# Kernel tuning notes

Hardware: AMD Instinct MI355X
Metric: run time of the kernel (lower is better)

The kernel has to match this reference:

```python
import jax, jax.numpy as jnp
import numpy as np

B, C, H, W = 1, 128, 48, 48
HC = 32                     # head_channel
NH = C // HC                # num heads = 4
K = 16                      # n_clusters
N = H * W                   # 2304
SCALE = HC ** 0.5
EPS = 1e-6


def setup_inputs() -> dict:
    key = jax.random.key(0)
    ks = jax.random.split(key, 20)
    s = 0.05  # weight init scale ~ xavier-ish for C=128
    def g(i, shape, sc=s):
        return jax.random.normal(ks[i], shape, dtype=jnp.float32) * sc
    return {
        'q_img': g(0, (B, C, H, W), 1.0),
        'k_img_map': g(1, (B, C, H, W), 1.0),
        'v_img_map': g(2, (B, C, H, W), 1.0),
        'pixel_coefficients': jax.random.uniform(ks[3], (B, N, N), dtype=jnp.float32),
        'labels': jax.random.randint(ks[4], (B, H, W), 0, K),
        # projections (stored as [in, out]; y = x @ w + b)
        'wq': g(5, (C, C)), 'bq': jnp.zeros((C,), jnp.float32),
        'wk': g(6, (C, C)), 'bk': jnp.zeros((C,), jnp.float32),
        'wv': g(7, (C, C)), 'bv': jnp.zeros((C,), jnp.float32),
        # mlp_1: Linear(C,2C) -> LeakyReLU(0.01) -> Linear(2C,C) (dropout=0 -> identity)
        'w1a': g(8, (C, 2 * C)), 'b1a': jnp.zeros((2 * C,), jnp.float32),
        'w1b': g(9, (2 * C, C)), 'b1b': jnp.zeros((C,), jnp.float32),
        # mlp_2
        'w2a': g(10, (C, 2 * C)), 'b2a': jnp.zeros((2 * C,), jnp.float32),
        'w2b': g(11, (2 * C, C)), 'b2b': jnp.zeros((C,), jnp.float32),
    }


def _mlp(x, wa, ba, wb, bb):
    h = x @ wa + ba
    h = jax.nn.leaky_relu(h, negative_slope=0.01)
    return h @ wb + bb


def reference(q_img, k_img_map, v_img_map, pixel_coefficients,
              wq, bq, wk, bk, wv, bv,
              w1a, b1a, w1b, b1b, w2a, b2a, w2b, b2b,
              labels):
    # projections on channel-last pixels
    q = q_img.transpose(0, 2, 3, 1).reshape(B, N, C) @ wq + bq
    k = k_img_map.transpose(0, 2, 3, 1).reshape(B, N, C) @ wk + bk
    v = v_img_map.transpose(0, 2, 3, 1).reshape(B, N, C) @ wv + bv

    labels_flat = labels.reshape(B, N)
    onehot = jax.nn.one_hot(labels_flat, K, dtype=q.dtype)        # [B,N,K]
    num_k = jnp.einsum('bnk,bnc->bkc', onehot, k)                 # [B,K,C]
    den_k = onehot.sum(axis=1)[:, :, None] + EPS                  # [B,K,1]
    centers_k = num_k / den_k

    qm = q.reshape(B, N, NH, HC).transpose(0, 2, 1, 3)            # [B,h,N,d]
    km = k.reshape(B, N, NH, HC).transpose(0, 2, 1, 3)
    vm = v.reshape(B, N, NH, HC).transpose(0, 2, 1, 3)
    kcm = centers_k.reshape(B, K, NH, HC).transpose(0, 2, 1, 3)   # [B,h,K,d]

    attn_intra = jnp.einsum('bhid,bhjd->bhij', qm, km)            # [B,h,N,N]
    attn_centers = jnp.einsum('bhid,bhkd->bhik', qm, kcm)         # [B,h,N,K]

    # gather center score per key's cluster: attn_centers[b,h,i,labels[b,j]]
    idx = jnp.broadcast_to(labels_flat[:, None, None, :], (B, NH, N, N))
    attn_inter = jnp.take_along_axis(attn_centers, idx, axis=3)   # [B,h,N,N]
    attn_inter = attn_inter * pixel_coefficients[:, None, :, :]

    same = labels_flat[:, None, :, None] == labels_flat[:, None, None, :]  # [B,1,N,N]
    scores = jnp.where(same, attn_intra, attn_inter) / SCALE
    attn_w = jax.nn.softmax(scores, axis=-1)

    out = jnp.einsum('bhij,bhjd->bhid', attn_w, vm)
    out = out.transpose(0, 2, 1, 3).reshape(B, N, C)              # [B,N,C]

    v_spatial = v.reshape(B, H, W, C).transpose(0, 3, 1, 2)       # [B,C,H,W]
    rs1 = v_spatial + _mlp(out, w1a, b1a, w1b, b1b).transpose(0, 2, 1).reshape(B, C, H, W)
    rs1_flat = rs1.transpose(0, 2, 3, 1).reshape(B, N, C)
    rs2 = rs1 + _mlp(rs1_flat, w2a, b2a, w2b, b2b).transpose(0, 2, 1).reshape(B, C, H, W)
    return rs2
```

## Files before the change

### kernel.cpp

```cpp
#include <hip/hip_runtime.h>
#include <hip/hip_bf16.h>
#include <math.h>

#define NPIX 2304
#define CCH  128
#define NH   4
#define HC   32
#define NCL  16
#define KSPLIT 8
#define KEYS 288
#define NSTEP 9
#define QSCALE 0.25503489f
#define PPT  16

typedef __attribute__((ext_vector_type(8))) short short8;
typedef __attribute__((ext_vector_type(4))) short short4v;
typedef __attribute__((ext_vector_type(4))) float f32x4;

#if __has_builtin(__builtin_amdgcn_exp2f)
#define EXP2(x) __builtin_amdgcn_exp2f(x)
#else
#define EXP2(x) __expf((x) * 0.6931471805599453f)
#endif

static __device__ __forceinline__ short f2bf(float x) {
    __hip_bfloat16 b = __float2bfloat16(x);
    return *reinterpret_cast<short*>(&b);
}

__global__ void __launch_bounds__(256) pack_w_kernel(
        const float* __restrict__ wq,  const float* __restrict__ wk,
        const float* __restrict__ wv,
        const float* __restrict__ w1a, const float* __restrict__ w1b,
        const float* __restrict__ w2a, const float* __restrict__ w2b,
        float4* __restrict__ pq,  float4* __restrict__ pk,
        float4* __restrict__ pv,
        short* __restrict__ t1a, short* __restrict__ t1b,
        short* __restrict__ t2a, short* __restrict__ t2b) {
    const int idx = blockIdx.x * 256 + threadIdx.x;
    if (idx < 12288) {
        const int which = idx >> 12, local = idx & 4095;
        const float* src = (which == 0) ? wq : (which == 1) ? wk : wv;
        float4*      dst = (which == 0) ? pq : (which == 1) ? pk : pv;
        const int g = local >> 7, o = local & 127;
        float4 v;
        v.x = src[(4 * g + 0) * 128 + o];
        v.y = src[(4 * g + 1) * 128 + o];
        v.z = src[(4 * g + 2) * 128 + o];
        v.w = src[(4 * g + 3) * 128 + o];
        dst[local] = v;
    } else {
        const int i2 = idx - 12288;
        const int which = i2 >> 12, local = i2 & 4095;
        short8 s;
        if (which == 0 || which == 2) {
            const float* src = (which == 0) ? w1a : w2a;
            short*       dst = (which == 0) ? t1a : t2a;
            const int o = local >> 4, g = local & 15;
#pragma unroll
            for (int j = 0; j < 8; ++j) s[j] = f2bf(src[(g * 8 + j) * 256 + o]);
            *(short8*)(dst + (size_t)o * 128 + g * 8) = s;
        } else {
            const float* src = (which == 1) ? w1b : w2b;
            short*       dst = (which == 1) ? t1b : t2b;
            const int o = local >> 5, g = local & 31;
#pragma unroll
            for (int j = 0; j < 8; ++j) s[j] = f2bf(src[(g * 8 + j) * 128 + o]);
            *(short8*)(dst + (size_t)o * 256 + g * 8) = s;
        }
    }
}

__global__ void __launch_bounds__(256) proj_kernel(
        const float* __restrict__ xq, const float* __restrict__ xk,
        const float* __restrict__ xv, const int* __restrict__ labels,
        const float4* __restrict__ pq, const float* __restrict__ bq,
        const float4* __restrict__ pk, const float* __restrict__ bk,
        const float4* __restrict__ pv, const float* __restrict__ bv,
        short* __restrict__ qbf, short* __restrict__ kbf,
        float* __restrict__ vbuf, short* __restrict__ vbfT,
        float* __restrict__ cpart, float* __restrict__ denpart) {
    __shared__ float xsP[CCH * PPT];
    __shared__ float ls2[2 * NCL * CCH];
    __shared__ float smls[32];
    const int which = blockIdx.y;
    const int pxblk = blockIdx.x;
    const int n0    = pxblk * PPT;
    const int t  = threadIdx.x;
    const int c  = t & 127;
    const int ph = t >> 7;
    const float*  x  = (which == 0) ? xq : (which == 1) ? xk : xv;
    const float4* wp = (which == 0) ? pq : (which == 1) ? pk : pv;
    const float*  b  = (which == 0) ? bq : (which == 1) ? bk : bv;

#pragma unroll
    for (int it = 0; it < 8; ++it) {
        const int flat = it * 256 + t;
        const int cc = flat >> 4;
        const int p  = flat & 15;
        xsP[flat] = x[cc * NPIX + n0 + p];
    }
    if (which == 1)
        for (int u = t; u < 2 * NCL * CCH; u += 256) ls2[u] = 0.f;
    __syncthreads();

    float acc[8];
    const float bb = b[c];
#pragma unroll
    for (int p = 0; p < 8; ++p) acc[p] = bb;

    for (int g = 0; g < CCH / 4; ++g) {
        const float4 w4 = wp[g * 128 + c];
#pragma unroll
        for (int j = 0; j < 4; ++j) {
            const float wv_ = (j == 0) ? w4.x : (j == 1) ? w4.y : (j == 2) ? w4.z : w4.w;
            const float4 xa = *(const float4*)(xsP + (4 * g + j) * PPT + ph * 8);
            const float4 xb = *(const float4*)(xsP + (4 * g + j) * PPT + ph * 8 + 4);
            acc[0] = fmaf(xa.x, wv_, acc[0]); acc[1] = fmaf(xa.y, wv_, acc[1]);
            acc[2] = fmaf(xa.z, wv_, acc[2]); acc[3] = fmaf(xa.w, wv_, acc[3]);
            acc[4] = fmaf(xb.x, wv_, acc[4]); acc[5] = fmaf(xb.y, wv_, acc[5]);
            acc[6] = fmaf(xb.z, wv_, acc[6]); acc[7] = fmaf(xb.w, wv_, acc[7]);
        }
    }

    const int nb = n0 + ph * 8;
    if (which == 0) {
#pragma unroll
        for (int p = 0; p < 8; ++p)
            qbf[(size_t)(nb + p) * CCH + c] = f2bf(acc[p] * QSCALE);
    } else if (which == 1) {
#pragma unroll
        for (int p = 0; p < 8; ++p)
            kbf[(size_t)(nb + p) * CCH + c] = f2bf(acc[p]);
        int lab8[8];
#pragma unroll
        for (int p = 0; p < 8; ++p) lab8[p] = labels[nb + p];
#pragma unroll
        for (int p = 0; p < 8; ++p)
            ls2[(ph * NCL + lab8[p]) * CCH + c] += acc[p];
        if (t < 32) {
            const int g2 = t >> 4, cl = t & 15;
            int cnt = 0;
#pragma unroll
            for (int p = 0; p < 8; ++p)
                cnt += (labels[n0 + g2 * 8 + p] == cl) ? 1 : 0;
            smls[t] = (float)cnt;
        }
        __syncthreads();
        for (int u = t; u < NCL * CCH; u += 256)
            cpart[(size_t)pxblk * 2048 + u] = ls2[u] + ls2[2048 + u];
        if (t < 16)
            denpart[pxblk * 16 + t] = smls[t] + smls[16 + t];
    } else {
#pragma unroll
        for (int p = 0; p < 8; ++p) vbuf[(size_t)(nb + p) * CCH + c] = acc[p];
        short8 s0;
#pragma unroll
        for (int p = 0; p < 8; ++p) s0[p] = f2bf(acc[p]);
        *(short8*)(vbfT + (size_t)c * NPIX + nb) = s0;
    }
}

__global__ void centersB_kernel(const float* __restrict__ cpart,
                                const float* __restrict__ denpart,
                                short* __restrict__ cbf) {
    const int idx = blockIdx.x * 256 + threadIdx.x;
    const int kk  = idx >> 7;
    float den = 0.f, s = 0.f;
    for (int b = 0; b < 144; ++b) den += denpart[b * 16 + kk];
    for (int b = 0; b < 144; ++b) s   += cpart[(size_t)b * 2048 + idx];
    cbf[idx] = f2bf(s / (den + 1e-6f));
}

__global__ void __launch_bounds__(256, 4) attn_part_kernel(
        const short* __restrict__ qbf,  const short* __restrict__ kbf,
        const short* __restrict__ vbfT, const short* __restrict__ cbf,
        const int* __restrict__ labels, const float* __restrict__ pc,
        float* __restrict__ part_o, float* __restrict__ part_l) {
    __shared__ __align__(16) short Pl[NH][16 * 40];
    __shared__ __align__(16) float aclT[NH][16][16];
    __shared__ int   labl[KEYS];
    const int qt   = blockIdx.x;
    const int ks   = blockIdx.y;
    const int tid  = threadIdx.x;
    const int w    = tid >> 6;
    const int lane = tid & 63;
    const int quad = lane >> 4;
    const int lq   = lane & 15;
    const int i0   = qt * 16;
    const int j0   = ks * KEYS;

    for (int u = tid; u < KEYS / 4; u += 256)
        *(int4*)(labl + u * 4) = *(const int4*)(labels + j0 + u * 4);

    const short8 aq = *(const short8*)(qbf + (size_t)(i0 + lq) * CCH + w * HC + quad * 8);
    {
        const short8 bc = *(const short8*)(cbf + (size_t)lq * CCH + w * HC + quad * 8);
        f32x4 z = {0.f, 0.f, 0.f, 0.f};
        f32x4 acd = __builtin_amdgcn_mfma_f32_16x16x32_bf16(aq, bc, z, 0, 0, 0);
        *(f32x4*)(&aclT[w][lq][quad * 4]) = acd;
    }
    int labi[4];
#pragma unroll
    for (int r = 0; r < 4; ++r) labi[r] = labels[i0 + quad * 4 + r];

    __syncthreads();

    const short* kp  = kbf  + (size_t)(j0 + lq) * CCH + w * HC + quad * 8;
    const short* vp  = vbfT + (size_t)(w * HC + lq) * NPIX + j0 + quad * 8;
    const float* pcp = pc   + (size_t)(i0 + quad * 4) * NPIX + j0 + lq;

    short8 k0A, k1A, v0A, v1A, k0B, k1B, v0B, v1B;
    float pcA[8], pcB[8];
    f32x4 accO0 = {0.f, 0.f, 0.f, 0.f};
    f32x4 accO1 = {0.f, 0.f, 0.f, 0.f};
    float lp[4] = {0.f, 0.f, 0.f, 0.f};

#define ISSUE(K0_, K1_, V0_, V1_, s) do {                                         \
        K0_ = *(const short8*)(kp + (size_t)(s) * 32 * CCH);                      \
        K1_ = *(const short8*)(kp + (size_t)((s) * 32 + 16) * CCH);               \
        V0_ = *(const short8*)(vp + (s) * 32);                                    \
        V1_ = *(const short8*)(vp + (size_t)16 * NPIX + (s) * 32);                \
    } while (0)

#define ISSUE_PC(dst, s) do {                                                     \
        _Pragma("unroll")                                                         \
        for (int r_ = 0; r_ < 4; ++r_) {                                          \
            dst[r_ * 2 + 0] = pcp[(size_t)r_ * NPIX + (s) * 32];                  \
            dst[r_ * 2 + 1] = pcp[(size_t)r_ * NPIX + (s) * 32 + 16];             \
        }                                                                         \
    } while (0)

#define COMPUTE(s, K0_, K1_, V0_, V1_, PCUSE) do {                                \
        _Pragma("unroll")                                                         \
        for (int kh = 0; kh < 2; ++kh) {                                          \
            const short8 bk = (kh == 0) ? K0_ : K1_;                              \
            f32x4 z = {0.f, 0.f, 0.f, 0.f};                                       \
            const f32x4 sv = __builtin_amdgcn_mfma_f32_16x16x32_bf16(aq, bk, z, 0, 0, 0);\
            const int slab = labl[(s) * 32 + kh * 16 + lq];                       \
            const f32x4 av4 = *(const f32x4*)(&aclT[w][slab][quad * 4]);          \
            _Pragma("unroll")                                                     \
            for (int r = 0; r < 4; ++r) {                                         \
                const float sc_ = (slab == labi[r]) ? sv[r] : av4[r] * PCUSE[r * 2 + kh];\
                const float p   = EXP2(sc_);                                      \
                lp[r] += p;                                                       \
                Pl[w][(quad * 4 + r) * 40 + kh * 16 + lq] = f2bf(p);              \
            }                                                                     \
        }                                                                         \
        const short8 ap = *(const short8*)(&Pl[w][lq * 40 + quad * 8]);           \
        accO0 = __builtin_amdgcn_mfma_f32_16x16x32_bf16(ap, V0_, accO0, 0, 0, 0); \
        accO1 = __builtin_amdgcn_mfma_f32_16x16x32_bf16(ap, V1_, accO1, 0, 0, 0); \
    } while (0)

    ISSUE(k0A, k1A, v0A, v1A, 0);
    ISSUE_PC(pcA, 0);
    for (int sb = 0; sb < NSTEP; sb += 2) {
        if (sb + 1 < NSTEP) { ISSUE(k0B, k1B, v0B, v1B, sb + 1); ISSUE_PC(pcB, sb + 1); }
        COMPUTE(sb, k0A, k1A, v0A, v1A, pcA);
        if (sb + 1 < NSTEP) {
            if (sb + 2 < NSTEP) { ISSUE(k0A, k1A, v0A, v1A, sb + 2); ISSUE_PC(pcA, sb + 2); }
            COMPUTE(sb + 1, k0B, k1B, v0B, v1B, pcB);
        }
    }
#undef ISSUE
#undef ISSUE_PC
#undef COMPUTE

#pragma unroll
    for (int r = 0; r < 4; ++r) {
        float v = lp[r];
        v += __shfl_xor(v, 1, 64);
        v += __shfl_xor(v, 2, 64);
        v += __shfl_xor(v, 4, 64);
        v += __shfl_xor(v, 8, 64);
        lp[r] = v;
    }
    if (lq == 0) {
#pragma unroll
        for (int r = 0; r < 4; ++r)
            part_l[((size_t)ks * NPIX + i0 + quad * 4 + r) * NH + w] = lp[r];
    }
#pragma unroll
    for (int r = 0; r < 4; ++r) {
        float* po = part_o + ((size_t)ks * NPIX + i0 + quad * 4 + r) * CCH + w * HC;
        po[lq]      = accO0[r];
        po[16 + lq] = accO1[r];
    }
}

#define XS 136
#define HS 264
__global__ void __launch_bounds__(256) mlp_mfma_kernel(
        const float* __restrict__ part_o, const float* __restrict__ part_l,
        const float* __restrict__ vbuf,
        const short* __restrict__ t1a, const float* __restrict__ b1a,
        const short* __restrict__ t1b, const float* __restrict__ b1b,
        const short* __restrict__ t2a, const float* __restrict__ b2a,
        const short* __restrict__ t2b, const float* __restrict__ b2b,
        float* __restrict__ outp) {
    __shared__ __align__(16) short xbf[16 * XS];
    __shared__ __align__(16) short hbf[16 * HS];
    __shared__ __align__(16) short r1bf[16 * XS];
    __shared__ float fT[128 * 20];
    const int n0 = blockIdx.x * 16;
    const int t  = threadIdx.x;
    const int w  = t >> 6, lane = t & 63, quad = lane >> 4, lq = lane & 15;

    for (int u = t; u < 512; u += 256) {
        const int p = u >> 5, c4 = (u & 31) * 4, hh = c4 >> 5;
        float ls_ = 0.f;
#pragma unroll
        for (int ks = 0; ks < KSPLIT; ++ks)
            ls_ += part_l[((size_t)ks * NPIX + n0 + p) * NH + hh];
        float sx = 0.f, sy = 0.f, sz = 0.f, sw2 = 0.f;
#pragma unroll
        for (int ks = 0; ks < KSPLIT; ++ks) {
            const float4 v = *(const float4*)(part_o + ((size_t)ks * NPIX + n0 + p) * CCH + c4);
            sx += v.x; sy += v.y; sz += v.z; sw2 += v.w;
        }
        const float inv = 1.f / ls_;
        short4v s;
        s[0] = f2bf(sx * inv); s[1] = f2bf(sy * inv);
        s[2] = f2bf(sz * inv); s[3] = f2bf(sw2 * inv);
        *(short4v*)(xbf + p * XS + c4) = s;
    }
    __syncthreads();

    {
        short8 a[4];
#pragma unroll
        for (int ks = 0; ks < 4; ++ks)
            a[ks] = *(const short8*)(xbf + lq * XS + ks * 32 + quad * 8);
#pragma unroll
        for (int tile = 0; tile < 4; ++tile) {
            const int out0 = w * 64 + tile * 16;
            f32x4 acc = {0.f, 0.f, 0.f, 0.f};
#pragma unroll
            for (int ks = 0; ks < 4; ++ks) {
                const short8 b = *(const short8*)(t1a + (size_t)(out0 + lq) * 128 + ks * 32 + quad * 8);
                acc = __builtin_amdgcn_mfma_f32_16x16x32_bf16(a[ks], b, acc, 0, 0, 0);
            }
            const float bb = b1a[out0 + lq];
#pragma unroll
            for (int r = 0; r < 4; ++r) {
                float v = acc[r] + bb;
                v = (v > 0.f) ? v : 0.01f * v;
                hbf[(quad * 4 + r) * HS + out0 + lq] = f2bf(v);
            }
        }
    }
    __syncthreads();

    float rs1f[2][4];
    {
        short8 a[8];
#pragma unroll
        for (int ks = 0; ks < 8; ++ks)
            a[ks] = *(const short8*)(hbf + lq * HS + ks * 32 + quad * 8);
#pragma unroll
        for (int tile = 0; tile < 2; ++tile) {
            const int out0 = w * 32 + tile * 16;
            f32x4 acc = {0.f, 0.f, 0.f, 0.f};
#pragma unroll
            for (int ks = 0; ks < 8; ++ks) {
                const short8 b = *(const short8*)(t1b + (size_t)(out0 + lq) * 256 + ks * 32 + quad * 8);
                acc = __builtin_amdgcn_mfma_f32_16x16x32_bf16(a[ks], b, acc, 0, 0, 0);
            }
            const float bb = b1b[out0 + lq];
#pragma unroll
            for (int r = 0; r < 4; ++r) {
                const float v = acc[r] + bb +
                    vbuf[(size_t)(n0 + quad * 4 + r) * CCH + out0 + lq];
                rs1f[tile][r] = v;
                r1bf[(quad * 4 + r) * XS + out0 + lq] = f2bf(v);
            }
        }
    }
    __syncthreads();

    {
        short8 a[4];
#pragma unroll
        for (int ks = 0; ks < 4; ++ks)
            a[ks] = *(const short8*)(r1bf + lq * XS + ks * 32 + quad * 8);
#pragma unroll
        for (int tile = 0; tile < 4; ++tile) {
            const int out0 = w * 64 + tile * 16;
            f32x4 acc = {0.f, 0.f, 0.f, 0.f};
#pragma unroll
            for (int ks = 0; ks < 4; ++ks) {
                const short8 b = *(const short8*)(t2a + (size_t)(out0 + lq) * 128 + ks * 32 + quad * 8);
                acc = __builtin_amdgcn_mfma_f32_16x16x32_bf16(a[ks], b, acc, 0, 0, 0);
            }
            const float bb = b2a[out0 + lq];
#pragma unroll
            for (int r = 0; r < 4; ++r) {
                float v = acc[r] + bb;
                v = (v > 0.f) ? v : 0.01f * v;
                hbf[(quad * 4 + r) * HS + out0 + lq] = f2bf(v);
            }
        }
    }
    __syncthreads();

    {
        short8 a[8];
#pragma unroll
        for (int ks = 0; ks < 8; ++ks)
            a[ks] = *(const short8*)(hbf + lq * HS + ks * 32 + quad * 8);
#pragma unroll
        for (int tile = 0; tile < 2; ++tile) {
            const int out0 = w * 32 + tile * 16;
            f32x4 acc = {0.f, 0.f, 0.f, 0.f};
#pragma unroll
            for (int ks = 0; ks < 8; ++ks) {
                const short8 b = *(const short8*)(t2b + (size_t)(out0 + lq) * 256 + ks * 32 + quad * 8);
                acc = __builtin_amdgcn_mfma_f32_16x16x32_bf16(a[ks], b, acc, 0, 0, 0);
            }
            const float bb = b2b[out0 + lq];
#pragma unroll
            for (int r = 0; r < 4; ++r)
                fT[(out0 + lq) * 20 + quad * 4 + r] = acc[r] + bb + rs1f[tile][r];
        }
    }
    __syncthreads();

    for (int u = t; u < 512; u += 256) {
        const int row = u >> 2, seg = u & 3;
        const float4 v = *(const float4*)(fT + row * 20 + seg * 4);
        *(float4*)(outp + (size_t)row * NPIX + n0 + seg * 4) = v;
    }
}

extern "C" void kernel_launch(void* const* d_in, const int* in_sizes, int n_in,
                              void* d_out, int out_size, void* d_ws, size_t ws_size,
                              hipStream_t stream) {
    const float* q_img = (const float*)d_in[0];
    const float* k_img = (const float*)d_in[1];
    const float* v_img = (const float*)d_in[2];
    const float* pc    = (const float*)d_in[3];
    const int*   labels= (const int*)  d_in[4];
    const float* wq = (const float*)d_in[5];   const float* bq = (const float*)d_in[6];
    const float* wk = (const float*)d_in[7];   const float* bk = (const float*)d_in[8];
    const float* wv = (const float*)d_in[9];   const float* bv = (const float*)d_in[10];
    const float* w1a = (const float*)d_in[11]; const float* b1a = (const float*)d_in[12];
    const float* w1b = (const float*)d_in[13]; const float* b1b = (const float*)d_in[14];
    const float* w2a = (const float*)d_in[15]; const float* b2a = (const float*)d_in[16];
    const float* w2b = (const float*)d_in[17]; const float* b2b = (const float*)d_in[18];

    float* fw = (float*)d_ws;
    float* vbuf    = fw;
    float* part_o  = vbuf + (size_t)NPIX * CCH;
    float* part_l  = part_o + (size_t)KSPLIT * NPIX * CCH;
    float* cpart   = part_l + (size_t)KSPLIT * NPIX * NH;
    float* denpart = cpart + (size_t)144 * 2048;
    float4* pq  = (float4*)(denpart + 144 * 16);
    float4* pk4 = pq + 4096;
    float4* pv4 = pk4 + 4096;
    short* t1a  = (short*)(pv4 + 4096);
    short* t1b  = t1a + 32768;
    short* t2a  = t1b + 32768;
    short* t2b  = t2a + 32768;
    short* qbf  = t2b + 32768;
    short* kbf  = qbf + (size_t)NPIX * CCH;
    short* vbfT = kbf + (size_t)NPIX * CCH;
    short* cbf  = vbfT + (size_t)NPIX * CCH;

    pack_w_kernel<<<112, 256, 0, stream>>>(
        wq, wk, wv, w1a, w1b, w2a, w2b, pq, pk4, pv4, t1a, t1b, t2a, t2b);
    proj_kernel<<<dim3(144, 3), 256, 0, stream>>>(
        q_img, k_img, v_img, labels, pq, bq, pk4, bk, pv4, bv,
        qbf, kbf, vbuf, vbfT, cpart, denpart);
    centersB_kernel<<<8, 256, 0, stream>>>(cpart, denpart, cbf);
    attn_part_kernel<<<dim3(144, KSPLIT), 256, 0, stream>>>(
        qbf, kbf, vbfT, cbf, labels, pc, part_o, part_l);
    mlp_mfma_kernel<<<144, 256, 0, stream>>>(
        part_o, part_l, vbuf, t1a, b1a, t1b, b1b, t2a, b2a, t2b, b2b,
        (float*)d_out);
}
```

Before: 157.5 us.

## Fold weight packing into projection kernel and widen MLP blocks to 1024 threads

The separate pack_w kernel goes away. Conversion of the MLP weights to bf16 now runs in an extra grid row (y==3) of the projection kernel, and the projection reads the fp32 q/k/v weights directly rather than a float4-repacked copy. The MLP kernel launches 1024 threads per block so each wave computes a single 16-wide output tile instead of looping over 2–4 tiles. The aim is to save a kernel launch and spread MLP work across more waves, at the cost of scalar weight loads in the projection and idle waves in the half-width MLP stages.

```diff
diff --git a/kernel.cpp b/kernel.cpp
--- a/kernel.cpp
+++ b/kernel.cpp
@@ -28,70 +28,56 @@
     return *reinterpret_cast<short*>(&b);
 }
 
-__global__ void __launch_bounds__(256) pack_w_kernel(
-        const float* __restrict__ wq,  const float* __restrict__ wk,
-        const float* __restrict__ wv,
-        const float* __restrict__ w1a, const float* __restrict__ w1b,
-        const float* __restrict__ w2a, const float* __restrict__ w2b,
-        float4* __restrict__ pq,  float4* __restrict__ pk,
-        float4* __restrict__ pv,
-        short* __restrict__ t1a, short* __restrict__ t1b,
-        short* __restrict__ t2a, short* __restrict__ t2b) {
-    const int idx = blockIdx.x * 256 + threadIdx.x;
-    if (idx < 12288) {
-        const int which = idx >> 12, local = idx & 4095;
-        const float* src = (which == 0) ? wq : (which == 1) ? wk : wv;
-        float4*      dst = (which == 0) ? pq : (which == 1) ? pk : pv;
-        const int g = local >> 7, o = local & 127;
-        float4 v;
-        v.x = src[(4 * g + 0) * 128 + o];
-        v.y = src[(4 * g + 1) * 128 + o];
-        v.z = src[(4 * g + 2) * 128 + o];
-        v.w = src[(4 * g + 3) * 128 + o];
-        dst[local] = v;
-    } else {
-        const int i2 = idx - 12288;
-        const int which = i2 >> 12, local = i2 & 4095;
-        short8 s;
-        if (which == 0 || which == 2) {
-            const float* src = (which == 0) ? w1a : w2a;
-            short*       dst = (which == 0) ? t1a : t2a;
-            const int o = local >> 4, g = local & 15;
-#pragma unroll
-            for (int j = 0; j < 8; ++j) s[j] = f2bf(src[(g * 8 + j) * 256 + o]);
-            *(short8*)(dst + (size_t)o * 128 + g * 8) = s;
-        } else {
-            const float* src = (which == 1) ? w1b : w2b;
-            short*       dst = (which == 1) ? t1b : t2b;
-            const int o = local >> 5, g = local & 31;
-#pragma unroll
-            for (int j = 0; j < 8; ++j) s[j] = f2bf(src[(g * 8 + j) * 128 + o]);
-            *(short8*)(dst + (size_t)o * 256 + g * 8) = s;
-        }
-    }
-}
-
 __global__ void __launch_bounds__(256) proj_kernel(
         const float* __restrict__ xq, const float* __restrict__ xk,
         const float* __restrict__ xv, const int* __restrict__ labels,
-        const float4* __restrict__ pq, const float* __restrict__ bq,
-        const float4* __restrict__ pk, const float* __restrict__ bk,
-        const float4* __restrict__ pv, const float* __restrict__ bv,
+        const float* __restrict__ wq, const float* __restrict__ bq,
+        const float* __restrict__ wk, const float* __restrict__ bk,
+        const float* __restrict__ wv, const float* __restrict__ bv,
+        const float* __restrict__ w1a, const float* __restrict__ w1b,
+        const float* __restrict__ w2a, const float* __restrict__ w2b,
         short* __restrict__ qbf, short* __restrict__ kbf,
         float* __restrict__ vbuf, short* __restrict__ vbfT,
-        float* __restrict__ cpart, float* __restrict__ denpart) {
+        float* __restrict__ cpart, float* __restrict__ denpart,
+        short* __restrict__ t1a, short* __restrict__ t1b,
+        short* __restrict__ t2a, short* __restrict__ t2b) {
     __shared__ float xsP[CCH * PPT];
     __shared__ float ls2[2 * NCL * CCH];
     __shared__ float smls[32];
     const int which = blockIdx.y;
     const int pxblk = blockIdx.x;
-    const int n0    = pxblk * PPT;
     const int t  = threadIdx.x;
+
+    if (which == 3) {
+        const int idx = pxblk * 256 + t;
+        if (idx < 16384) {
+            const int sel = idx >> 12, local = idx & 4095;
+            short8 s;
+            if (sel == 0 || sel == 2) {
+                const float* src = (sel == 0) ? w1a : w2a;
+                short*       dst = (sel == 0) ? t1a : t2a;
+                const int o = local >> 4, g = local & 15;
+#pragma unroll
+                for (int j = 0; j < 8; ++j) s[j] = f2bf(src[(g * 8 + j) * 256 + o]);
+                *(short8*)(dst + (size_t)o * 128 + g * 8) = s;
+            } else {
+                const float* src = (sel == 1) ? w1b : w2b;
+                short*       dst = (sel == 1) ? t1b : t2b;
+                const int o = local >> 5, g = local & 31;
+#pragma unroll
+                for (int j = 0; j < 8; ++j) s[j] = f2bf(src[(g * 8 + j) * 128 + o]);
+                *(short8*)(dst + (size_t)o * 256 + g * 8) = s;
+            }
+        }
+        return;
+    }
+
+    const int n0 = pxblk * PPT;
     const int c  = t & 127;
     const int ph = t >> 7;
-    const float*  x  = (which == 0) ? xq : (which == 1) ? xk : xv;
-    const float4* wp = (which == 0) ? pq : (which == 1) ? pk : pv;
-    const float*  b  = (which == 0) ? bq : (which == 1) ? bk : bv;
+    const float* x = (which == 0) ? xq : (which == 1) ? xk : xv;
+    const float* w = (which == 0) ? wq : (which == 1) ? wk : wv;
+    const float* b = (which == 0) ? bq : (which == 1) ? bk : bv;
 
 #pragma unroll
     for (int it = 0; it < 8; ++it) {
@@ -109,18 +95,15 @@
 #pragma unroll
     for (int p = 0; p < 8; ++p) acc[p] = bb;
 
-    for (int g = 0; g < CCH / 4; ++g) {
-        const float4 w4 = wp[g * 128 + c];
-#pragma unroll
-        for (int j = 0; j < 4; ++j) {
-            const float wv_ = (j == 0) ? w4.x : (j == 1) ? w4.y : (j == 2) ? w4.z : w4.w;
-            const float4 xa = *(const float4*)(xsP + (4 * g + j) * PPT + ph * 8);
-            const float4 xb = *(const float4*)(xsP + (4 * g + j) * PPT + ph * 8 + 4);
-            acc[0] = fmaf(xa.x, wv_, acc[0]); acc[1] = fmaf(xa.y, wv_, acc[1]);
-            acc[2] = fmaf(xa.z, wv_, acc[2]); acc[3] = fmaf(xa.w, wv_, acc[3]);
-            acc[4] = fmaf(xb.x, wv_, acc[4]); acc[5] = fmaf(xb.y, wv_, acc[5]);
-            acc[6] = fmaf(xb.z, wv_, acc[6]); acc[7] = fmaf(xb.w, wv_, acc[7]);
-        }
+#pragma unroll 4
+    for (int in = 0; in < CCH; ++in) {
+        const float wv_ = w[in * CCH + c];
+        const float4 xa = *(const float4*)(xsP + in * PPT + ph * 8);
+        const float4 xb = *(const float4*)(xsP + in * PPT + ph * 8 + 4);
+        acc[0] = fmaf(xa.x, wv_, acc[0]); acc[1] = fmaf(xa.y, wv_, acc[1]);
+        acc[2] = fmaf(xa.z, wv_, acc[2]); acc[3] = fmaf(xa.w, wv_, acc[3]);
+        acc[4] = fmaf(xb.x, wv_, acc[4]); acc[5] = fmaf(xb.y, wv_, acc[5]);
+        acc[6] = fmaf(xb.z, wv_, acc[6]); acc[7] = fmaf(xb.w, wv_, acc[7]);
     }
 
     const int nb = n0 + ph * 8;
@@ -290,7 +273,7 @@
 
 #define XS 136
 #define HS 264
-__global__ void __launch_bounds__(256) mlp_mfma_kernel(
+__global__ void __launch_bounds__(1024) mlp_mfma_kernel(
         const float* __restrict__ part_o, const float* __restrict__ part_l,
         const float* __restrict__ vbuf,
         const short* __restrict__ t1a, const float* __restrict__ b1a,
@@ -306,8 +289,8 @@
     const int t  = threadIdx.x;
     const int w  = t >> 6, lane = t & 63, quad = lane >> 4, lq = lane & 15;
 
-    for (int u = t; u < 512; u += 256) {
-        const int p = u >> 5, c4 = (u & 31) * 4, hh = c4 >> 5;
+    if (t < 512) {
+        const int p = t >> 5, c4 = (t & 31) * 4, hh = c4 >> 5;
         float ls_ = 0.f;
 #pragma unroll
         for (int ks = 0; ks < KSPLIT; ++ks)
@@ -331,49 +314,43 @@
 #pragma unroll
         for (int ks = 0; ks < 4; ++ks)
             a[ks] = *(const short8*)(xbf + lq * XS + ks * 32 + quad * 8);
-#pragma unroll
-        for (int tile = 0; tile < 4; ++tile) {
-            const int out0 = w * 64 + tile * 16;
-            f32x4 acc = {0.f, 0.f, 0.f, 0.f};
-#pragma unroll
-            for (int ks = 0; ks < 4; ++ks) {
-                const short8 b = *(const short8*)(t1a + (size_t)(out0 + lq) * 128 + ks * 32 + quad * 8);
-                acc = __builtin_amdgcn_mfma_f32_16x16x32_bf16(a[ks], b, acc, 0, 0, 0);
-            }
-            const float bb = b1a[out0 + lq];
-#pragma unroll
-            for (int r = 0; r < 4; ++r) {
-                float v = acc[r] + bb;
-                v = (v > 0.f) ? v : 0.01f * v;
-                hbf[(quad * 4 + r) * HS + out0 + lq] = f2bf(v);
-            }
-        }
-    }
-    __syncthreads();
-
-    float rs1f[2][4];
-    {
+        const int out0 = w * 16;
+        f32x4 acc = {0.f, 0.f, 0.f, 0.f};
+#pragma unroll
+        for (int ks = 0; ks < 4; ++ks) {
+            const short8 b = *(const short8*)(t1a + (size_t)(out0 + lq) * 128 + ks * 32 + quad * 8);
+            acc = __builtin_amdgcn_mfma_f32_16x16x32_bf16(a[ks], b, acc, 0, 0, 0);
+        }
+        const float bb = b1a[out0 + lq];
+#pragma unroll
+        for (int r = 0; r < 4; ++r) {
+            float v = acc[r] + bb;
+            v = (v > 0.f) ? v : 0.01f * v;
+            hbf[(quad * 4 + r) * HS + out0 + lq] = f2bf(v);
+        }
+    }
+    __syncthreads();
+
+    float rs1f[4];
+    if (w < 8) {
         short8 a[8];
 #pragma unroll
         for (int ks = 0; ks < 8; ++ks)
             a[ks] = *(const short8*)(hbf + lq * HS + ks * 32 + quad * 8);
-#pragma unroll
-        for (int tile = 0; tile < 2; ++tile) {
-            const int out0 = w * 32 + tile * 16;
-            f32x4 acc = {0.f, 0.f, 0.f, 0.f};
-#pragma unroll
-            for (int ks = 0; ks < 8; ++ks) {
-                const short8 b = *(const short8*)(t1b + (size_t)(out0 + lq) * 256 + ks * 32 + quad * 8);
-                acc = __builtin_amdgcn_mfma_f32_16x16x32_bf16(a[ks], b, acc, 0, 0, 0);
-            }
-            const float bb = b1b[out0 + lq];
-#pragma unroll
-            for (int r = 0; r < 4; ++r) {
-                const float v = acc[r] + bb +
-                    vbuf[(size_t)(n0 + quad * 4 + r) * CCH + out0 + lq];
-                rs1f[tile][r] = v;
-                r1bf[(quad * 4 + r) * XS + out0 + lq] = f2bf(v);
-            }
+        const int out0 = w * 16;
+        f32x4 acc = {0.f, 0.f, 0.f, 0.f};
+#pragma unroll
+        for (int ks = 0; ks < 8; ++ks) {
+            const short8 b = *(const short8*)(t1b + (size_t)(out0 + lq) * 256 + ks * 32 + quad * 8);
+            acc = __builtin_amdgcn_mfma_f32_16x16x32_bf16(a[ks], b, acc, 0, 0, 0);
+        }
+        const float bb = b1b[out0 + lq];
+#pragma unroll
+        for (int r = 0; r < 4; ++r) {
+            const float v = acc[r] + bb +
+                vbuf[(size_t)(n0 + quad * 4 + r) * CCH + out0 + lq];
+            rs1f[r] = v;
+            r1bf[(quad * 4 + r) * XS + out0 + lq] = f2bf(v);
         }
     }
     __syncthreads();
@@ -383,50 +360,44 @@
 #pragma unroll
         for (int ks = 0; ks < 4; ++ks)
             a[ks] = *(const short8*)(r1bf + lq * XS + ks * 32 + quad * 8);
-#pragma unroll
-        for (int tile = 0; tile < 4; ++tile) {
-            const int out0 = w * 64 + tile * 16;
-            f32x4 acc = {0.f, 0.f, 0.f, 0.f};
-#pragma unroll
-            for (int ks = 0; ks < 4; ++ks) {
-                const short8 b = *(const short8*)(t2a + (size_t)(out0 + lq) * 128 + ks * 32 + quad * 8);
-                acc = __builtin_amdgcn_mfma_f32_16x16x32_bf16(a[ks], b, acc, 0, 0, 0);
-            }
-            const float bb = b2a[out0 + lq];
-#pragma unroll
-            for (int r = 0; r < 4; ++r) {
-                float v = acc[r] + bb;
-                v = (v > 0.f) ? v : 0.01f * v;
-                hbf[(quad * 4 + r) * HS + out0 + lq] = f2bf(v);
-            }
-        }
-    }
-    __syncthreads();
-
-    {
+        const int out0 = w * 16;
+        f32x4 acc = {0.f, 0.f, 0.f, 0.f};
+#pragma unroll
+        for (int ks = 0; ks < 4; ++ks) {
+            const short8 b = *(const short8*)(t2a + (size_t)(out0 + lq) * 128 + ks * 32 + quad * 8);
+            acc = __builtin_amdgcn_mfma_f32_16x16x32_bf16(a[ks], b, acc, 0, 0, 0);
+        }
+        const float bb = b2a[out0 + lq];
+#pragma unroll
+        for (int r = 0; r < 4; ++r) {
+            float v = acc[r] + bb;
+            v = (v > 0.f) ? v : 0.01f * v;
+            hbf[(quad * 4 + r) * HS + out0 + lq] = f2bf(v);
+        }
+    }
+    __syncthreads();
+
+    if (w < 8) {
         short8 a[8];
 #pragma unroll
         for (int ks = 0; ks < 8; ++ks)
             a[ks] = *(const short8*)(hbf + lq * HS + ks * 32 + quad * 8);
-#pragma unroll
-        for (int tile = 0; tile < 2; ++tile) {
-            const int out0 = w * 32 + tile * 16;
-            f32x4 acc = {0.f, 0.f, 0.f, 0.f};
-#pragma unroll
-            for (int ks = 0; ks < 8; ++ks) {
-                const short8 b = *(const short8*)(t2b + (size_t)(out0 + lq) * 256 + ks * 32 + quad * 8);
-                acc = __builtin_amdgcn_mfma_f32_16x16x32_bf16(a[ks], b, acc, 0, 0, 0);
-            }
-            const float bb = b2b[out0 + lq];
-#pragma unroll
-            for (int r = 0; r < 4; ++r)
-                fT[(out0 + lq) * 20 + quad * 4 + r] = acc[r] + bb + rs1f[tile][r];
-        }
-    }
-    __syncthreads();
-
-    for (int u = t; u < 512; u += 256) {
-        const int row = u >> 2, seg = u & 3;
+        const int out0 = w * 16;
+        f32x4 acc = {0.f, 0.f, 0.f, 0.f};
+#pragma unroll
+        for (int ks = 0; ks < 8; ++ks) {
+            const short8 b = *(const short8*)(t2b + (size_t)(out0 + lq) * 256 + ks * 32 + quad * 8);
+            acc = __builtin_amdgcn_mfma_f32_16x16x32_bf16(a[ks], b, acc, 0, 0, 0);
+        }
+        const float bb = b2b[out0 + lq];
+#pragma unroll
+        for (int r = 0; r < 4; ++r)
+            fT[(out0 + lq) * 20 + quad * 4 + r] = acc[r] + bb + rs1f[r];
+    }
+    __syncthreads();
+
+    if (t < 512) {
+        const int row = t >> 2, seg = t & 3;
         const float4 v = *(const float4*)(fT + row * 20 + seg * 4);
         *(float4*)(outp + (size_t)row * NPIX + n0 + seg * 4) = v;
     }
@@ -454,10 +425,7 @@
     float* part_l  = part_o + (size_t)KSPLIT * NPIX * CCH;
     float* cpart   = part_l + (size_t)KSPLIT * NPIX * NH;
     float* denpart = cpart + (size_t)144 * 2048;
-    float4* pq  = (float4*)(denpart + 144 * 16);
-    float4* pk4 = pq + 4096;
-    float4* pv4 = pk4 + 4096;
-    short* t1a  = (short*)(pv4 + 4096);
+    short* t1a  = (short*)(denpart + 144 * 16);
     short* t1b  = t1a + 32768;
     short* t2a  = t1b + 32768;
     short* t2b  = t2a + 32768;
@@ -466,15 +434,14 @@
     short* vbfT = kbf + (size_t)NPIX * CCH;
     short* cbf  = vbfT + (size_t)NPIX * CCH;
 
-    pack_w_kernel<<<112, 256, 0, stream>>>(
-        wq, wk, wv, w1a, w1b, w2a, w2b, pq, pk4, pv4, t1a, t1b, t2a, t2b);
-    proj_kernel<<<dim3(144, 3), 256, 0, stream>>>(
-        q_img, k_img, v_img, labels, pq, bq, pk4, bk, pv4, bv,
-        qbf, kbf, vbuf, vbfT, cpart, denpart);
+    proj_kernel<<<dim3(144, 4), 256, 0, stream>>>(
+        q_img, k_img, v_img, labels, wq, bq, wk, bk, wv, bv,
+        w1a, w1b, w2a, w2b,
+        qbf, kbf, vbuf, vbfT, cpart, denpart, t1a, t1b, t2a, t2b);
     centersB_kernel<<<8, 256, 0, stream>>>(cpart, denpart, cbf);
     attn_part_kernel<<<dim3(144, KSPLIT), 256, 0, stream>>>(
         qbf, kbf, vbfT, cbf, labels, pc, part_o, part_l);
-    mlp_mfma_kernel<<<144, 256, 0, stream>>>(
+    mlp_mfma_kernel<<<144, 1024, 0, stream>>>(
         part_o, part_l, vbuf, t1a, b1a, t1b, b1b, t2a, b2a, t2b, b2b,
         (float*)d_out);
 }
```

Result: no change. 159.2 us (+1.1%).
